# Kernel optimization log

Hardware: AMD Instinct MI355X
Metric: run time of the kernel (lower is better)

## Reference

```python
import jax, jax.numpy as jnp
import numpy as np
from jax import lax

THRESHOLD = 10.0  # p-norm threshold in HSEM
BN_EPS = 1e-5
DN = ('NCHW', 'OIHW', 'NCHW')


def setup_inputs() -> dict:
    key = jax.random.key(0)
    ks = jax.random.split(key, 9)
    b, c, h, w = 2, 256, 64, 64
    c_out = 512
    # scale x so pairwise L2 distances straddle the threshold (dense-ish hypergraph)
    x = jax.random.normal(ks[0], (b, c, h, w), dtype=jnp.float32) * 0.4
    fc_w = jax.random.normal(ks[1], (c, c), dtype=jnp.float32) * 0.02
    fc_b = jax.random.normal(ks[2], (c,), dtype=jnp.float32) * 0.02
    bn_gamma = jnp.ones((c,), dtype=jnp.float32)
    bn_beta = jnp.zeros((c,), dtype=jnp.float32)
    down_w = jax.random.normal(ks[3], (c, c, 3, 3), dtype=jnp.float32) * 0.02
    down_b = jax.random.normal(ks[4], (c,), dtype=jnp.float32) * 0.02
    out_w = jax.random.normal(ks[5], (c_out, c, 1, 1), dtype=jnp.float32) * 0.02
    out_b = jax.random.normal(ks[6], (c_out,), dtype=jnp.float32) * 0.02
    return {"x": x, "fc_w": fc_w, "fc_b": fc_b, "bn_gamma": bn_gamma,
            "bn_beta": bn_beta, "down_w": down_w, "down_b": down_b,
            "out_w": out_w, "out_b": out_b}


def _mean_agg(path, X):
    # path: [b, n_tgt, n_src], X: [b, n_src, d]; mean aggregation with inf->0 masking
    s = jnp.sum(path, axis=2, keepdims=True)           # [b, n_tgt, 1]
    norm = jnp.where(s > 0, 1.0 / jnp.where(s > 0, s, 1.0), 0.0)
    return norm * jnp.matmul(path, X)


def reference(x, fc_w, fc_b, bn_gamma, bn_beta, down_w, down_b, out_w, out_b):
    b, c, h, w = x.shape
    n = h * w
    xf = x.reshape(b, c, n).transpose(0, 2, 1)          # [b, n, c]
    # cdist (euclidean): ||a-b|| via expansion
    sq = jnp.sum(xf * xf, axis=-1)                      # [b, n]
    d2 = sq[:, :, None] + sq[:, None, :] - 2.0 * jnp.einsum('bnc,bmc->bnm', xf, xf)
    dist = jnp.sqrt(jnp.maximum(d2, 0.0))               # [b, n, n]
    hg = (dist < THRESHOLD).astype(x.dtype)             # dynamic hypergraph incidence
    # HyPConv: fc -> v2e (H^T) -> e2v (H)
    y = jnp.einsum('bnc,dc->bnd', xf, fc_w) + fc_b      # Linear(c1, c2)
    E = _mean_agg(jnp.swapaxes(hg, 1, 2), y)            # vertex -> edge
    v = _mean_agg(hg, E)                                # edge -> vertex
    xf = v + xf                                         # residual
    x4 = xf.transpose(0, 2, 1).reshape(b, c, h, w)
    # BatchNorm2d (training-mode batch statistics, biased var)
    mean = jnp.mean(x4, axis=(0, 2, 3))
    var = jnp.var(x4, axis=(0, 2, 3))
    xn = (x4 - mean[None, :, None, None]) * lax.rsqrt(var + BN_EPS)[None, :, None, None]
    xn = xn * bn_gamma[None, :, None, None] + bn_beta[None, :, None, None]
    xa = xn * jax.nn.sigmoid(xn)                        # SiLU
    # Downsample: pad (right=1, bottom=1) then 3x3 stride-2 VALID conv
    xp = jnp.pad(xa, ((0, 0), (0, 0), (0, 1), (0, 1)))
    xd = lax.conv_general_dilated(xp, down_w, (2, 2), 'VALID', dimension_numbers=DN)
    xd = xd + down_b[None, :, None, None]
    out = lax.conv_general_dilated(xd, out_w, (1, 1), 'VALID', dimension_numbers=DN)
    out = out + out_b[None, :, None, None]
    return out
```

## Files before the change

### kernel.cpp

```cpp
#include <hip/hip_runtime.h>
#include <hip/hip_bf16.h>
#include <math.h>

#define NPIX 4096
#define CH   256

#define OFF_XP    0u
#define OFF_XR    1048576u
#define OFF_VB    2097152u
#define OFF_TBS   3145728u
#define OFF_TBS2  4194304u
#define OFF_HG    5242880u
#define OFF_SQ    6291456u
#define OFF_PART  6299648u
#define OFF_BNSS  6365184u
#define OFF_DINV  6365696u
#define OFF_W3P   6373888u
#define OFF_WFCP  6668800u
#define OFF_WOUTP 6701568u

typedef __attribute__((ext_vector_type(8))) short bf16x8;
typedef __attribute__((ext_vector_type(16))) float f32x16;

static __device__ __forceinline__ short f2b(float f) {
  __hip_bfloat16 h = __float2bfloat16(f);
  return *reinterpret_cast<short*>(&h);
}
static __device__ __forceinline__ float b2f(short s) {
  union { unsigned u; float f; } r;
  r.u = ((unsigned)(unsigned short)s) << 16;
  return r.f;
}

static __device__ __forceinline__ bf16x8 byte2bf(unsigned byte) {
  union { unsigned u[4]; bf16x8 h; } r;
  r.u[0] = ((byte * 0x8001u) & 0x10001u) * 0x3F80u;
  r.u[1] = (((byte >> 2) * 0x8001u) & 0x10001u) * 0x3F80u;
  r.u[2] = (((byte >> 4) * 0x8001u) & 0x10001u) * 0x3F80u;
  r.u[3] = (((byte >> 6) * 0x8001u) & 0x10001u) * 0x3F80u;
  return r.h;
}

static __device__ __forceinline__ size_t packoff(int m, int c) {
  return ((size_t)((m >> 5) * 16 + (c >> 4)) * 2 + ((c >> 3) & 1)) * 256 + (m & 31) * 8 + (c & 7);
}

__global__ __launch_bounds__(256) void k_front(const float* __restrict__ x,
                                               short* __restrict__ xp,
                                               float* __restrict__ sq) {
  __shared__ float lds[256][33];
  __shared__ float red2[8][32];
  const int b = blockIdx.y;
  const int n0 = blockIdx.x * 32;
  const int t = threadIdx.x;
  const float* xb = x + (size_t)b * CH * NPIX + n0;
  const int j = t & 31, cg8 = t >> 5;
#pragma unroll 4
  for (int it = 0; it < 32; ++it) {
    const int c = it * 8 + cg8;
    lds[c][j] = xb[(size_t)c * NPIX + j];
  }
  __syncthreads();
  {
    const int n = t & 31, cg = t >> 5;
    float s = 0.f;
#pragma unroll 8
    for (int i = 0; i < 32; ++i) {
      const float v = lds[cg * 32 + i][n];
      s += v * v;
    }
    red2[cg][n] = s;
  }
  short* xpb = xp + (size_t)b * NPIX * CH;
#pragma unroll
  for (int i = 0; i < 4; ++i) {
    const int f = i * 256 + t;
    const int n = f & 31, c0 = (f >> 5) * 8;
    short tmp[8];
#pragma unroll
    for (int k = 0; k < 8; ++k) tmp[k] = f2b(lds[c0 + k][n]);
    short* dst = xpb + packoff(n0 + n, c0);
    *(short4*)dst = *(short4*)&tmp[0];
    *(short4*)(dst + 4) = *(short4*)&tmp[4];
  }
  __syncthreads();
  if (t < 32) {
    float s = 0.f;
#pragma unroll
    for (int cg = 0; cg < 8; ++cg) s += red2[cg][t];
    sq[b * NPIX + n0 + t] = s;
  }
}

__global__ void k_packall(const float* __restrict__ fc_w, const float* __restrict__ ow,
                          const float* __restrict__ dw, short* __restrict__ wfcp,
                          short* __restrict__ woutp, short* __restrict__ w3p) {
  const int i = blockIdx.x * 256 + threadIdx.x;
  if (i < 65536) {
    wfcp[packoff(i >> 8, i & 255)] = f2b(fc_w[i]);
  } else if (i < 196608) {
    const int j = i - 65536;
    woutp[packoff(j >> 8, j & 255)] = f2b(ow[j]);
  } else {
    const int j = i - 196608;
    const int oc = j / 2304;
    const int rem = j % 2304;
    const int c = rem / 9, tap = rem % 9;
    const size_t off = ((size_t)((tap * 8 + (oc >> 5)) * 16 + (c >> 4)) * 2 + ((c >> 3) & 1)) * 256
                     + (oc & 31) * 8 + (c & 7);
    w3p[off] = f2b(dw[j]);
  }
}

__global__ __launch_bounds__(256) void k_gram2(const short* __restrict__ xp,
                                               const float* __restrict__ sq,
                                               unsigned* __restrict__ hgbit) {
  const int b = blockIdx.z;
  int tt = blockIdx.x;
  int bi = (int)((65.0f - sqrtf(4225.0f - 8.0f * (float)tt)) * 0.5f);
  bi = bi < 0 ? 0 : (bi > 31 ? 31 : bi);
  while (bi * (65 - bi) / 2 > tt) --bi;
  while ((bi + 1) * (64 - bi) / 2 <= tt) ++bi;
  const int bj = bi + (tt - bi * (65 - bi) / 2);
  const int i0 = bi * 128, j0 = bj * 128;

  const int t = threadIdx.x;
  const int lane = t & 63, wid = t >> 6;
  const int wm = wid >> 1, wn = wid & 1;
  const int c = lane & 31, h = lane >> 5;
  const short* xb = xp + (size_t)b * NPIX * CH;
  const int ibase = i0 + wm * 64;
  const int jbase = j0 + wn * 64;

  f32x16 acc[2][2];
#pragma unroll
  for (int m = 0; m < 2; ++m)
#pragma unroll
    for (int n = 0; n < 2; ++n)
#pragma unroll
      for (int r = 0; r < 16; ++r) acc[m][n][r] = 0.f;

  const short* pa = xb + (size_t)(ibase >> 5) * 8192 + lane * 8;
  const short* pb = xb + (size_t)(jbase >> 5) * 8192 + lane * 8;

#pragma unroll 4
  for (int kb = 0; kb < 16; ++kb) {
    const bf16x8 a0 = *(const bf16x8*)(pa + kb * 512);
    const bf16x8 a1 = *(const bf16x8*)(pa + 8192 + kb * 512);
    const bf16x8 b0 = *(const bf16x8*)(pb + kb * 512);
    const bf16x8 b1 = *(const bf16x8*)(pb + 8192 + kb * 512);
    acc[0][0] = __builtin_amdgcn_mfma_f32_32x32x16_bf16(a0, b0, acc[0][0], 0, 0, 0);
    acc[0][1] = __builtin_amdgcn_mfma_f32_32x32x16_bf16(a0, b1, acc[0][1], 0, 0, 0);
    acc[1][0] = __builtin_amdgcn_mfma_f32_32x32x16_bf16(a1, b0, acc[1][0], 0, 0, 0);
    acc[1][1] = __builtin_amdgcn_mfma_f32_32x32x16_bf16(a1, b1, acc[1][1], 0, 0, 0);
  }

  const int sqb = b * NPIX;
#pragma unroll
  for (int m = 0; m < 2; ++m) {
    float4 sqa[4];
#pragma unroll
    for (int q = 0; q < 4; ++q)
      sqa[q] = *(const float4*)(sq + sqb + ibase + m * 32 + q * 8 + 4 * h);
#pragma unroll
    for (int n = 0; n < 2; ++n) {
      const float sj = sq[sqb + jbase + n * 32 + c];
      const int wj = (jbase + n * 32) >> 5;
#pragma unroll
      for (int q = 0; q < 4; ++q) {
        const float sqq[4] = {sqa[q].x, sqa[q].y, sqa[q].z, sqa[q].w};
#pragma unroll
        for (int rr = 0; rr < 4; ++rr) {
          const int reg = q * 4 + rr;
          const float d2 = sqq[rr] + sj - 2.f * acc[m][n][reg];
          const unsigned long long bal = __ballot(d2 < 100.f);
          if ((lane & 31) == reg) {
            const int row = ibase + m * 32 + rr + 8 * q + 4 * h;
            const unsigned wd = h ? (unsigned)(bal >> 32) : (unsigned)bal;
            hgbit[(size_t)(sqb + row) * 128 + wj] = wd;
          }
        }
      }
    }
  }
}

__global__ void k_mirror(unsigned* __restrict__ hg) {
  const int b = blockIdx.y;
  const int g = threadIdx.x >> 5;
  const int r = threadIdx.x & 31;
  const int tile = blockIdx.x * 8 + g;
  const int ta = tile >> 7, tb = tile & 127;
  if ((ta >> 2) <= (tb >> 2)) return;
  unsigned* H = hg + (size_t)b * NPIX * 128;
  unsigned w = H[(size_t)(tb * 32 + r) * 128 + ta];
#pragma unroll
  for (int s = 16; s >= 1; s >>= 1) {
    const unsigned M = (s == 16) ? 0xFFFF0000u : (s == 8) ? 0xFF00FF00u :
                       (s == 4) ? 0xF0F0F0F0u : (s == 2) ? 0xCCCCCCCCu : 0xAAAAAAAAu;
    const unsigned p = __shfl_xor(w, s, 32);
    w = (r & s) ? ((w & M) | ((p >> s) & ~M)) : ((w & ~M) | ((p << s) & M));
  }
  H[(size_t)(ta * 32 + r) * 128 + tb] = w;
}

__global__ void k_dinv(const unsigned* __restrict__ hg, float* __restrict__ dinvf) {
  const int row = blockIdx.x, l = threadIdx.x;
  const unsigned w0 = hg[(size_t)row * 128 + l * 2];
  const unsigned w1 = hg[(size_t)row * 128 + l * 2 + 1];
  int n = __popc(w0) + __popc(w1);
#pragma unroll
  for (int off = 32; off; off >>= 1) n += __shfl_down(n, off);
  if (l == 0) dinvf[row] = 1.0f / (float)n;
}

__global__ __launch_bounds__(256) void k_mfma_fc2(const short* __restrict__ wfcp,
                                                  const short* __restrict__ xp,
                                                  short* __restrict__ C,
                                                  const float* __restrict__ bias) {
  const int b = blockIdx.z;
  xp += (size_t)b * NPIX * CH;
  C += (size_t)b << 20;
  const int t = threadIdx.x, l = t & 63, wid = t >> 6;
  const int m0 = blockIdx.y * 128 + wid * 32, n0 = blockIdx.x * 64;
  const int col = l & 31, half = l >> 5;
  f32x16 acc[2];
#pragma unroll
  for (int nt = 0; nt < 2; ++nt)
#pragma unroll
    for (int r = 0; r < 16; ++r) acc[nt][r] = 0.f;
  const short* pa = wfcp + (size_t)(m0 >> 5) * 8192 + l * 8;
  const short* pb = xp + (size_t)(n0 >> 5) * 8192 + l * 8;
#pragma unroll 4
  for (int kb = 0; kb < 16; ++kb) {
    const bf16x8 a = *(const bf16x8*)(pa + kb * 512);
    const bf16x8 b0 = *(const bf16x8*)(pb + kb * 512);
    const bf16x8 b1 = *(const bf16x8*)(pb + 8192 + kb * 512);
    acc[0] = __builtin_amdgcn_mfma_f32_32x32x16_bf16(a, b0, acc[0], 0, 0, 0);
    acc[1] = __builtin_amdgcn_mfma_f32_32x32x16_bf16(a, b1, acc[1], 0, 0, 0);
  }
  const int cb = m0 >> 5;
#pragma unroll
  for (int nt = 0; nt < 2; ++nt) {
    const int node = n0 + nt * 32 + col;
    short* dst = C + ((size_t)cb * 512 + (node >> 3)) * 256 + (node & 7);
#pragma unroll
    for (int q = 0; q < 4; ++q)
#pragma unroll
      for (int rr = 0; rr < 4; ++rr) {
        const int c31 = rr + 8 * q + 4 * half;
        dst[c31 * 8] = f2b(acc[nt][q * 4 + rr] + bias[m0 + c31]);
      }
  }
}

__global__ __launch_bounds__(256) void k_hgemm_t3(const short* __restrict__ tbs,
                                                  const unsigned* __restrict__ hg,
                                                  const float* __restrict__ dinvf,
                                                  short* __restrict__ tbs2) {
  __shared__ float red[4][64][33];
  const int b = blockIdx.z;
  const int n0 = blockIdx.x * 32;
  const int cbp = blockIdx.y;
  const int ks = threadIdx.x >> 6;
  const int l = threadIdx.x & 63;
  const int col = l & 31, half = l >> 5;
  const int sh8 = half * 8;

  f32x16 acc0, acc1;
#pragma unroll
  for (int r = 0; r < 16; ++r) { acc0[r] = 0.f; acc1[r] = 0.f; }

  const short* pa0 = tbs + ((size_t)b << 20) + ((size_t)(cbp * 2) * 512 + half) * 256
                   + col * 8 + ks * 32768;
  const short* pa1 = pa0 + 131072;
  const uint4* hrow = (const uint4*)((const unsigned char*)hg
                    + ((size_t)b * NPIX + n0 + col) * 512 + ks * 128);

#pragma unroll 2
  for (int o = 0; o < 8; ++o) {
    const uint4 wq = hrow[o];
    const unsigned ww[4] = {wq.x, wq.y, wq.z, wq.w};
#pragma unroll
    for (int s = 0; s < 4; ++s) {
      const unsigned wb = ww[s];
      const bf16x8 a00 = *(const bf16x8*)(pa0);
      const bf16x8 a01 = *(const bf16x8*)(pa0 + 512);
      const bf16x8 a10 = *(const bf16x8*)(pa1);
      const bf16x8 a11 = *(const bf16x8*)(pa1 + 512);
      pa0 += 1024; pa1 += 1024;
      const bf16x8 b0 = byte2bf((wb >> sh8) & 0xFFu);
      const bf16x8 b1 = byte2bf((wb >> (16 + sh8)) & 0xFFu);
      acc0 = __builtin_amdgcn_mfma_f32_32x32x16_bf16(a00, b0, acc0, 0, 0, 0);
      acc0 = __builtin_amdgcn_mfma_f32_32x32x16_bf16(a01, b1, acc0, 0, 0, 0);
      acc1 = __builtin_amdgcn_mfma_f32_32x32x16_bf16(a10, b0, acc1, 0, 0, 0);
      acc1 = __builtin_amdgcn_mfma_f32_32x32x16_bf16(a11, b1, acc1, 0, 0, 0);
    }
  }

#pragma unroll
  for (int r = 0; r < 16; ++r) { red[ks][l][r] = acc0[r]; red[ks][l][16 + r] = acc1[r]; }
  __syncthreads();

  const int n = n0 + col;
  const float dinv = dinvf[b * NPIX + n];
  short* dst0 = tbs2 + ((size_t)b << 20) + ((size_t)(cbp * 2) * 512 + (n >> 3)) * 256 + (n & 7);
  short* dst1 = dst0 + 131072;
#pragma unroll
  for (int rj = 0; rj < 8; ++rj) {
    const int reg = ks * 8 + rj;
    const float s = red[0][l][reg] + red[1][l][reg] + red[2][l][reg] + red[3][l][reg];
    const int rm = reg & 15;
    const int c31 = (rm & 3) + 8 * (rm >> 2) + 4 * half;
    (reg < 16 ? dst0 : dst1)[c31 * 8] = f2b(s * dinv);
  }
}

__global__ __launch_bounds__(256) void k_hgemm_n3(const unsigned* __restrict__ hg,
                                                  const short* __restrict__ tbs2,
                                                  const float* __restrict__ dinvf,
                                                  const short* __restrict__ xp,
                                                  short* __restrict__ vb) {
  __shared__ float red[4][64][33];
  const int b = blockIdx.z;
  const int cbp = blockIdx.x;
  const int m0 = blockIdx.y * 32;
  const int ks = threadIdx.x >> 6;
  const int l = threadIdx.x & 63;
  const int col = l & 31, half = l >> 5;
  const int sh8 = half * 8;

  f32x16 acc0, acc1;
#pragma unroll
  for (int r = 0; r < 16; ++r) { acc0[r] = 0.f; acc1[r] = 0.f; }

  const short* pb0 = tbs2 + ((size_t)b << 20) + ((size_t)(cbp * 2) * 512 + half) * 256
                   + col * 8 + ks * 32768;
  const short* pb1 = pb0 + 131072;
  const uint4* hrow = (const uint4*)((const unsigned char*)hg
                    + ((size_t)b * NPIX + m0 + col) * 512 + ks * 128);

#pragma unroll 2
  for (int o = 0; o < 8; ++o) {
    const uint4 wq = hrow[o];
    const unsigned ww[4] = {wq.x, wq.y, wq.z, wq.w};
#pragma unroll
    for (int s = 0; s < 4; ++s) {
      const unsigned wb = ww[s];
      const bf16x8 b00 = *(const bf16x8*)(pb0);
      const bf16x8 b01 = *(const bf16x8*)(pb0 + 512);
      const bf16x8 b10 = *(const bf16x8*)(pb1);
      const bf16x8 b11 = *(const bf16x8*)(pb1 + 512);
      pb0 += 1024; pb1 += 1024;
      const bf16x8 a0 = byte2bf((wb >> sh8) & 0xFFu);
      const bf16x8 a1 = byte2bf((wb >> (16 + sh8)) & 0xFFu);
      acc0 = __builtin_amdgcn_mfma_f32_32x32x16_bf16(a0, b00, acc0, 0, 0, 0);
      acc0 = __builtin_amdgcn_mfma_f32_32x32x16_bf16(a1, b01, acc0, 0, 0, 0);
      acc1 = __builtin_amdgcn_mfma_f32_32x32x16_bf16(a0, b10, acc1, 0, 0, 0);
      acc1 = __builtin_amdgcn_mfma_f32_32x32x16_bf16(a1, b11, acc1, 0, 0, 0);
    }
  }

#pragma unroll
  for (int r = 0; r < 16; ++r) { red[ks][l][r] = acc0[r]; red[ks][l][16 + r] = acc1[r]; }
  __syncthreads();

  const short* xpb = xp + (size_t)b * NPIX * CH;
  const int cc = cbp * 64 + col;
#pragma unroll
  for (int rj = 0; rj < 8; ++rj) {
    const int reg = ks * 8 + rj;
    const float s = red[0][l][reg] + red[1][l][reg] + red[2][l][reg] + red[3][l][reg];
    const int rm = reg & 15;
    const int r = m0 + (rm & 3) + 8 * (rm >> 2) + 4 * half;
    const int ccc = cc + (reg < 16 ? 0 : 32);
    const size_t o = ((size_t)(b * NPIX + r)) * CH + ccc;
    const short xv = xpb[packoff(r, ccc)];
    vb[o] = f2b(s * dinvf[b * NPIX + r] + b2f(xv));
  }
}

__global__ void k_bnstat(const short* __restrict__ vb, float* __restrict__ part) {
  const int t = threadIdx.x, blk = blockIdx.x;
  float s = 0.f, ss = 0.f;
  const short* p = vb + (size_t)blk * 64 * CH;
  for (int r = 0; r < 64; ++r) {
    const float v = b2f(p[r * CH + t]);
    s += v; ss += v * v;
  }
  part[blk * 512 + t] = s;
  part[blk * 512 + 256 + t] = ss;
}

__global__ void k_bnfin(const float* __restrict__ part, const float* __restrict__ gamma,
                        const float* __restrict__ beta, float* __restrict__ bnss) {
  const int t = threadIdx.x;
  float s = 0.f, ss = 0.f;
  for (int i = 0; i < 128; ++i) { s += part[i * 512 + t]; ss += part[i * 512 + 256 + t]; }
  const float mean = s * (1.f / 8192.f);
  const float var = ss * (1.f / 8192.f) - mean * mean;
  const float inv = rsqrtf(var + 1e-5f);
  const float sc = gamma[t] * inv;
  bnss[t] = sc;
  bnss[256 + t] = beta[t] - mean * sc;
}

__global__ void k_bnapply3(const short* __restrict__ vb, const float* __restrict__ bnss,
                           short* __restrict__ xpp) {
  const int i = blockIdx.x * 256 + threadIdx.x;
  const short4 sv = reinterpret_cast<const short4*>(vb)[i];
  const int c0 = (i & 63) * 4;
  const int n = (i >> 6) & 4095;
  const int b = i >> 18;
  const float4 sc = *(const float4*)(bnss + c0);
  const float4 sh = *(const float4*)(bnss + 256 + c0);
  const float u0 = b2f(sv.x) * sc.x + sh.x;
  const float u1 = b2f(sv.y) * sc.y + sh.y;
  const float u2 = b2f(sv.z) * sc.z + sh.z;
  const float u3 = b2f(sv.w) * sc.w + sh.w;
  short4 o;
  o.x = f2b(u0 / (1.f + expf(-u0)));
  o.y = f2b(u1 / (1.f + expf(-u1)));
  o.z = f2b(u2 / (1.f + expf(-u2)));
  o.w = f2b(u3 / (1.f + expf(-u3)));
  const int ih = n >> 6, iw = n & 63;
  const int p = iw & 1, ow = iw >> 1;
  const size_t off = ((size_t)(((b * 2 + p) * 64 + ih) * 16 + (c0 >> 4)) * 2 + ((c0 >> 3) & 1)) * 256
                   + ow * 8 + (c0 & 7);
  *(short4*)(xpp + off) = o;
}

__global__ __launch_bounds__(64) void k_conv4(const short* __restrict__ xpp,
                                              const short* __restrict__ w3p,
                                              float* __restrict__ convp) {
  const int ocg = blockIdx.x;
  const int oh = blockIdx.y;
  const int bz = blockIdx.z;
  const int b = bz >> 1, kh2 = bz & 1;
  const int l = threadIdx.x;
  const int col = l & 31;
  const bf16x8 zv = {0, 0, 0, 0, 0, 0, 0, 0};

  f32x16 acc;
#pragma unroll
  for (int r = 0; r < 16; ++r) acc[r] = 0.f;

  for (int kh = 0; kh < 3; ++kh) {
    const int ih = 2 * oh + kh;
    if (ih >= 64) continue;
#pragma unroll
    for (int kw = 0; kw < 3; ++kw) {
      const int p = kw & 1;
      const short* pa = xpp + ((size_t)((b * 2 + p) * 64 + ih) * 16 + kh2 * 8) * 512
                      + l * 8 + (kw == 2 ? 8 : 0);
      const short* pb = w3p + ((size_t)((kh * 3 + kw) * 8 + ocg) * 16 + kh2 * 8) * 512 + l * 8;
      const bool kill = (kw == 2) && (col == 31);
#pragma unroll
      for (int kb = 0; kb < 8; ++kb) {
        bf16x8 a = *(const bf16x8*)(pa + kb * 512);
        if (kill) a = zv;
        const bf16x8 bb = *(const bf16x8*)(pb + kb * 512);
        acc = __builtin_amdgcn_mfma_f32_32x32x16_bf16(a, bb, acc, 0, 0, 0);
      }
    }
  }
  const int half = l >> 5;
  const int oc = ocg * 32 + col;
#pragma unroll
  for (int q = 0; q < 4; ++q)
#pragma unroll
    for (int rr = 0; rr < 4; ++rr) {
      const int ow = rr + 8 * q + 4 * half;
      convp[((size_t)(kh2 * 2 + b) * 1024 + oh * 32 + ow) * 256 + oc] = acc[q * 4 + rr];
    }
}

__global__ void k_convmerge2(const float* __restrict__ convp, const float* __restrict__ db,
                             short* __restrict__ xdtb) {
  const int i = blockIdx.x * 256 + threadIdx.x;
  const int b = i >> 16, px = (i >> 6) & 1023, oc0 = (i & 63) * 4;
  const float4 h0 = *(const float4*)(convp + ((size_t)b * 1024 + px) * 256 + oc0);
  const float4 h1 = *(const float4*)(convp + ((size_t)(2 + b) * 1024 + px) * 256 + oc0);
  const float4 bv = *(const float4*)(db + oc0);
  short4 o;
  o.x = f2b(h0.x + h1.x + bv.x);
  o.y = f2b(h0.y + h1.y + bv.y);
  o.z = f2b(h0.z + h1.z + bv.z);
  o.w = f2b(h0.w + h1.w + bv.w);
  const size_t off = ((size_t)((b * 32 + (px >> 5)) * 16 + (oc0 >> 4)) * 2 + ((oc0 >> 3) & 1)) * 256
                   + (px & 31) * 8 + (oc0 & 7);
  *(short4*)(xdtb + off) = o;
}

__global__ __launch_bounds__(256) void k_mfma_nt2(const short* __restrict__ woutp,
                                                  const short* __restrict__ xdtb,
                                                  float* __restrict__ C,
                                                  const float* __restrict__ bias) {
  const int b = blockIdx.z;
  xdtb += (size_t)b * 1024 * CH;
  C += (size_t)b * 512 * 1024;
  const int t = threadIdx.x, l = t & 63, wid = t >> 6;
  const int m0 = blockIdx.y * 128 + wid * 32, n0 = blockIdx.x * 64;
  const int col = l & 31, half = l >> 5;
  f32x16 acc[2];
#pragma unroll
  for (int nt = 0; nt < 2; ++nt)
#pragma unroll
    for (int r = 0; r < 16; ++r) acc[nt][r] = 0.f;
  const short* pa = woutp + (size_t)(m0 >> 5) * 8192 + l * 8;
  const short* pb = xdtb + (size_t)(n0 >> 5) * 8192 + l * 8;
#pragma unroll 4
  for (int kb = 0; kb < 16; ++kb) {
    const bf16x8 a = *(const bf16x8*)(pa + kb * 512);
    const bf16x8 b0 = *(const bf16x8*)(pb + kb * 512);
    const bf16x8 b1 = *(const bf16x8*)(pb + 8192 + kb * 512);
    acc[0] = __builtin_amdgcn_mfma_f32_32x32x16_bf16(a, b0, acc[0], 0, 0, 0);
    acc[1] = __builtin_amdgcn_mfma_f32_32x32x16_bf16(a, b1, acc[1], 0, 0, 0);
  }
#pragma unroll
  for (int nt = 0; nt < 2; ++nt) {
#pragma unroll
    for (int q = 0; q < 4; ++q)
#pragma unroll
      for (int rr = 0; rr < 4; ++rr) {
        const int row = m0 + rr + 8 * q + 4 * half;
        const int cc = n0 + nt * 32 + col;
        C[(size_t)row * 1024 + cc] = acc[nt][q * 4 + rr] + bias[row];
      }
  }
}

extern "C" void kernel_launch(void* const* d_in, const int* in_sizes, int n_in,
                              void* d_out, int out_size, void* d_ws, size_t ws_size,
                              hipStream_t stream) {
  const float* x     = (const float*)d_in[0];
  const float* fc_w  = (const float*)d_in[1];
  const float* fc_b  = (const float*)d_in[2];
  const float* gamma = (const float*)d_in[3];
  const float* beta  = (const float*)d_in[4];
  const float* dw    = (const float*)d_in[5];
  const float* db    = (const float*)d_in[6];
  const float* ow    = (const float*)d_in[7];
  const float* ob    = (const float*)d_in[8];

  float* ws   = (float*)d_ws;
  short* xp   = (short*)(ws + OFF_XP);
  float* convp= ws + OFF_XP;
  short* vb   = (short*)(ws + OFF_VB);
  short* tbs  = (short*)(ws + OFF_TBS);
  short* xdtb = (short*)(ws + OFF_TBS);
  short* tbs2 = (short*)(ws + OFF_TBS2);
  short* xpp  = (short*)(ws + OFF_TBS2);
  unsigned* hg = (unsigned*)(ws + OFF_HG);
  float* sqv  = ws + OFF_SQ;
  float* part = ws + OFF_PART;
  float* bnss = ws + OFF_BNSS;
  float* dinvf= ws + OFF_DINV;
  short* w3p  = (short*)(ws + OFF_W3P);
  short* wfcp = (short*)(ws + OFF_WFCP);
  short* woutp= (short*)(ws + OFF_WOUTP);
  float* out  = (float*)d_out;

  k_front<<<dim3(128, 2), 256, 0, stream>>>(x, xp, sqv);
  k_packall<<<3072, 256, 0, stream>>>(fc_w, ow, dw, wfcp, woutp, w3p);
  k_gram2<<<dim3(528, 1, 2), 256, 0, stream>>>(xp, sqv, hg);
  k_mirror<<<dim3(2048, 2), 256, 0, stream>>>(hg);
  k_mfma_fc2<<<dim3(64, 2, 2), 256, 0, stream>>>(wfcp, xp, tbs, fc_b);
  k_dinv<<<8192, 64, 0, stream>>>(hg, dinvf);
  k_hgemm_t3<<<dim3(128, 4, 2), 256, 0, stream>>>(tbs, hg, dinvf, tbs2);
  k_hgemm_n3<<<dim3(4, 128, 2), 256, 0, stream>>>(hg, tbs2, dinvf, xp, vb);
  k_bnstat<<<128, 256, 0, stream>>>(vb, part);
  k_bnfin<<<1, 256, 0, stream>>>(part, gamma, beta, bnss);
  k_bnapply3<<<2048, 256, 0, stream>>>(vb, bnss, xpp);
  k_conv4<<<dim3(8, 32, 4), 64, 0, stream>>>(xpp, w3p, convp);
  k_convmerge2<<<512, 256, 0, stream>>>(convp, db, xdtb);
  k_mfma_nt2<<<dim3(16, 4, 2), 256, 0, stream>>>(woutp, xdtb, out, ob);
}
```

Measured before the change: 144.0 us.

## Widen gram tiles to 128x256 and split conv channels four ways

The Gram/threshold kernel now computes 128x256 tiles per block over a rectangular-triangle tile schedule. Each wave holds a 2x4 grid of MFMA accumulators, so A-operand loads are reused across more columns and fewer blocks are launched. The 3x3 downsample conv splits input channels into four groups instead of two, doubling the number of blocks for more parallelism. The merge kernel then sums four partial buffers. The trade-offs are higher register pressure in the gram kernel and extra partial-sum traffic in the conv path.

```diff
diff --git a/kernel.cpp b/kernel.cpp
--- a/kernel.cpp
+++ b/kernel.cpp
@@ -112,17 +112,15 @@
   }
 }
 
-__global__ __launch_bounds__(256) void k_gram2(const short* __restrict__ xp,
-                                               const float* __restrict__ sq,
-                                               unsigned* __restrict__ hgbit) {
+__global__ __launch_bounds__(256, 2) void k_gram3(const short* __restrict__ xp,
+                                                  const float* __restrict__ sq,
+                                                  unsigned* __restrict__ hgbit) {
   const int b = blockIdx.z;
   int tt = blockIdx.x;
-  int bi = (int)((65.0f - sqrtf(4225.0f - 8.0f * (float)tt)) * 0.5f);
-  bi = bi < 0 ? 0 : (bi > 31 ? 31 : bi);
-  while (bi * (65 - bi) / 2 > tt) --bi;
-  while ((bi + 1) * (64 - bi) / 2 <= tt) ++bi;
-  const int bj = bi + (tt - bi * (65 - bi) / 2);
-  const int i0 = bi * 128, j0 = bj * 128;
+  int bi = 0;
+  while (true) { const int cnt = 16 - (bi >> 1); if (tt < cnt) break; tt -= cnt; ++bi; }
+  const int bj = (bi >> 1) + tt;
+  const int i0 = bi * 128, j0 = bj * 256;
 
   const int t = threadIdx.x;
   const int lane = t & 63, wid = t >> 6;
@@ -130,29 +128,31 @@
   const int c = lane & 31, h = lane >> 5;
   const short* xb = xp + (size_t)b * NPIX * CH;
   const int ibase = i0 + wm * 64;
-  const int jbase = j0 + wn * 64;
-
-  f32x16 acc[2][2];
+  const int jbase = j0 + wn * 128;
+
+  f32x16 acc[2][4];
 #pragma unroll
   for (int m = 0; m < 2; ++m)
 #pragma unroll
-    for (int n = 0; n < 2; ++n)
+    for (int n = 0; n < 4; ++n)
 #pragma unroll
       for (int r = 0; r < 16; ++r) acc[m][n][r] = 0.f;
 
   const short* pa = xb + (size_t)(ibase >> 5) * 8192 + lane * 8;
   const short* pb = xb + (size_t)(jbase >> 5) * 8192 + lane * 8;
 
-#pragma unroll 4
+#pragma unroll 2
   for (int kb = 0; kb < 16; ++kb) {
     const bf16x8 a0 = *(const bf16x8*)(pa + kb * 512);
     const bf16x8 a1 = *(const bf16x8*)(pa + 8192 + kb * 512);
-    const bf16x8 b0 = *(const bf16x8*)(pb + kb * 512);
-    const bf16x8 b1 = *(const bf16x8*)(pb + 8192 + kb * 512);
-    acc[0][0] = __builtin_amdgcn_mfma_f32_32x32x16_bf16(a0, b0, acc[0][0], 0, 0, 0);
-    acc[0][1] = __builtin_amdgcn_mfma_f32_32x32x16_bf16(a0, b1, acc[0][1], 0, 0, 0);
-    acc[1][0] = __builtin_amdgcn_mfma_f32_32x32x16_bf16(a1, b0, acc[1][0], 0, 0, 0);
-    acc[1][1] = __builtin_amdgcn_mfma_f32_32x32x16_bf16(a1, b1, acc[1][1], 0, 0, 0);
+    bf16x8 bb[4];
+#pragma unroll
+    for (int n = 0; n < 4; ++n) bb[n] = *(const bf16x8*)(pb + (size_t)n * 8192 + kb * 512);
+#pragma unroll
+    for (int n = 0; n < 4; ++n) {
+      acc[0][n] = __builtin_amdgcn_mfma_f32_32x32x16_bf16(a0, bb[n], acc[0][n], 0, 0, 0);
+      acc[1][n] = __builtin_amdgcn_mfma_f32_32x32x16_bf16(a1, bb[n], acc[1][n], 0, 0, 0);
+    }
   }
 
   const int sqb = b * NPIX;
@@ -163,7 +163,7 @@
     for (int q = 0; q < 4; ++q)
       sqa[q] = *(const float4*)(sq + sqb + ibase + m * 32 + q * 8 + 4 * h);
 #pragma unroll
-    for (int n = 0; n < 2; ++n) {
+    for (int n = 0; n < 4; ++n) {
       const float sj = sq[sqb + jbase + n * 32 + c];
       const int wj = (jbase + n * 32) >> 5;
 #pragma unroll
@@ -430,13 +430,13 @@
   *(short4*)(xpp + off) = o;
 }
 
-__global__ __launch_bounds__(64) void k_conv4(const short* __restrict__ xpp,
+__global__ __launch_bounds__(64) void k_conv5(const short* __restrict__ xpp,
                                               const short* __restrict__ w3p,
                                               float* __restrict__ convp) {
   const int ocg = blockIdx.x;
   const int oh = blockIdx.y;
   const int bz = blockIdx.z;
-  const int b = bz >> 1, kh2 = bz & 1;
+  const int b = bz & 1, cs = bz >> 1;
   const int l = threadIdx.x;
   const int col = l & 31;
   const bf16x8 zv = {0, 0, 0, 0, 0, 0, 0, 0};
@@ -451,12 +451,12 @@
 #pragma unroll
     for (int kw = 0; kw < 3; ++kw) {
       const int p = kw & 1;
-      const short* pa = xpp + ((size_t)((b * 2 + p) * 64 + ih) * 16 + kh2 * 8) * 512
+      const short* pa = xpp + ((size_t)((b * 2 + p) * 64 + ih) * 16 + cs * 4) * 512
                       + l * 8 + (kw == 2 ? 8 : 0);
-      const short* pb = w3p + ((size_t)((kh * 3 + kw) * 8 + ocg) * 16 + kh2 * 8) * 512 + l * 8;
+      const short* pb = w3p + ((size_t)((kh * 3 + kw) * 8 + ocg) * 16 + cs * 4) * 512 + l * 8;
       const bool kill = (kw == 2) && (col == 31);
 #pragma unroll
-      for (int kb = 0; kb < 8; ++kb) {
+      for (int kb = 0; kb < 4; ++kb) {
         bf16x8 a = *(const bf16x8*)(pa + kb * 512);
         if (kill) a = zv;
         const bf16x8 bb = *(const bf16x8*)(pb + kb * 512);
@@ -471,22 +471,25 @@
 #pragma unroll
     for (int rr = 0; rr < 4; ++rr) {
       const int ow = rr + 8 * q + 4 * half;
-      convp[((size_t)(kh2 * 2 + b) * 1024 + oh * 32 + ow) * 256 + oc] = acc[q * 4 + rr];
-    }
-}
-
-__global__ void k_convmerge2(const float* __restrict__ convp, const float* __restrict__ db,
+      convp[((size_t)bz * 1024 + oh * 32 + ow) * 256 + oc] = acc[q * 4 + rr];
+    }
+}
+
+__global__ void k_convmerge3(const float* __restrict__ convp, const float* __restrict__ db,
                              short* __restrict__ xdtb) {
   const int i = blockIdx.x * 256 + threadIdx.x;
   const int b = i >> 16, px = (i >> 6) & 1023, oc0 = (i & 63) * 4;
-  const float4 h0 = *(const float4*)(convp + ((size_t)b * 1024 + px) * 256 + oc0);
-  const float4 h1 = *(const float4*)(convp + ((size_t)(2 + b) * 1024 + px) * 256 + oc0);
+  const size_t base = ((size_t)px) * 256 + oc0;
+  const float4 h0 = *(const float4*)(convp + ((size_t)(0 + b) << 18) + base);
+  const float4 h1 = *(const float4*)(convp + ((size_t)(2 + b) << 18) + base);
+  const float4 h2 = *(const float4*)(convp + ((size_t)(4 + b) << 18) + base);
+  const float4 h3 = *(const float4*)(convp + ((size_t)(6 + b) << 18) + base);
   const float4 bv = *(const float4*)(db + oc0);
   short4 o;
-  o.x = f2b(h0.x + h1.x + bv.x);
-  o.y = f2b(h0.y + h1.y + bv.y);
-  o.z = f2b(h0.z + h1.z + bv.z);
-  o.w = f2b(h0.w + h1.w + bv.w);
+  o.x = f2b(h0.x + h1.x + h2.x + h3.x + bv.x);
+  o.y = f2b(h0.y + h1.y + h2.y + h3.y + bv.y);
+  o.z = f2b(h0.z + h1.z + h2.z + h3.z + bv.z);
+  o.w = f2b(h0.w + h1.w + h2.w + h3.w + bv.w);
   const size_t off = ((size_t)((b * 32 + (px >> 5)) * 16 + (oc0 >> 4)) * 2 + ((oc0 >> 3) & 1)) * 256
                    + (px & 31) * 8 + (oc0 & 7);
   *(short4*)(xdtb + off) = o;
@@ -563,7 +566,7 @@
 
   k_front<<<dim3(128, 2), 256, 0, stream>>>(x, xp, sqv);
   k_packall<<<3072, 256, 0, stream>>>(fc_w, ow, dw, wfcp, woutp, w3p);
-  k_gram2<<<dim3(528, 1, 2), 256, 0, stream>>>(xp, sqv, hg);
+  k_gram3<<<dim3(272, 1, 2), 256, 0, stream>>>(xp, sqv, hg);
   k_mirror<<<dim3(2048, 2), 256, 0, stream>>>(hg);
   k_mfma_fc2<<<dim3(64, 2, 2), 256, 0, stream>>>(wfcp, xp, tbs, fc_b);
   k_dinv<<<8192, 64, 0, stream>>>(hg, dinvf);
@@ -572,7 +575,7 @@
   k_bnstat<<<128, 256, 0, stream>>>(vb, part);
   k_bnfin<<<1, 256, 0, stream>>>(part, gamma, beta, bnss);
   k_bnapply3<<<2048, 256, 0, stream>>>(vb, bnss, xpp);
-  k_conv4<<<dim3(8, 32, 4), 64, 0, stream>>>(xpp, w3p, convp);
-  k_convmerge2<<<512, 256, 0, stream>>>(convp, db, xdtb);
+  k_conv5<<<dim3(8, 32, 8), 64, 0, stream>>>(xpp, w3p, convp);
+  k_convmerge3<<<512, 256, 0, stream>>>(convp, db, xdtb);
   k_mfma_nt2<<<dim3(16, 4, 2), 256, 0, stream>>>(woutp, xdtb, out, ob);
 }
```

After: 144.3 us. About the same (+0.2%).
